# Performance work log

Measured on AMD Instinct MI355X. Metric: run time of the kernel, lower is better.

Reference implementation:

```python
import jax, jax.numpy as jnp
import numpy as np
from jax import lax

VOCAB = 2048
HID = 1024
BATCH = 64
SEQ = 256

def setup_inputs() -> dict:
    key = jax.random.key(0)
    ks = jax.random.split(key, 6)
    s = 0.02
    return {
        "X": jax.random.randint(ks[0], (BATCH, SEQ), 0, VOCAB),
        # gate weights stacked as [f, i, o, c_tilde] along output dim (same math as 4 separate Linears)
        "W1": jax.random.normal(ks[1], (VOCAB + HID, 4 * HID), jnp.float32) * s,
        "b1": jnp.zeros((4 * HID,), jnp.float32),
        "W2": jax.random.normal(ks[2], (HID + HID, 4 * HID), jnp.float32) * s,
        "b2": jnp.zeros((4 * HID,), jnp.float32),
        "W3": jax.random.normal(ks[3], (HID + HID, 4 * HID), jnp.float32) * s,
        "b3": jnp.zeros((4 * HID,), jnp.float32),
        "Wout": jax.random.normal(ks[4], (HID, VOCAB), jnp.float32) * s,
        "bout": jnp.zeros((VOCAB,), jnp.float32),
    }

def _cell(x, h, c, W, b):
    # concat(x, h) @ [Wf|Wi|Wo|Wc] + b -> split into 4 gates
    g = jnp.concatenate([x, h], axis=1) @ W + b
    f, i, o, ct = jnp.split(g, 4, axis=1)
    c = jax.nn.sigmoid(f) * c + jax.nn.sigmoid(i) * jnp.tanh(ct)
    h = jax.nn.sigmoid(o) * jnp.tanh(c)
    return h, c

def reference(X, W1, b1, W2, b2, W3, b3, Wout, bout):
    Xoh = jax.nn.one_hot(X.T, VOCAB, dtype=jnp.float32)  # [T, B, V]
    z = jnp.zeros((BATCH, HID), jnp.float32)
    init = (z, z, z, z, z, z)

    def step(carry, x):
        h1, c1, h2, c2, h3, c3 = carry
        h1, c1 = _cell(x, h1, c1, W1, b1)
        h2, c2 = _cell(h1, h2, c2, W2, b2)
        h3, c3 = _cell(h2, h3, c3, W3, b3)
        y = h3 @ Wout + bout  # [B, V]
        return (h1, c1, h2, c2, h3, c3), y

    carry, ys = lax.scan(step, init, Xoh)
    out = ys.reshape(SEQ * BATCH, VOCAB)  # == torch.cat(outputs, dim=0)
    h1, c1, h2, c2, h3, c3 = carry
    return (out, h1, c1, h2, c2, h3, c3)
```

## Files before the change

kernel.cpp:

```cpp
#include <hip/hip_runtime.h>
#include <hip/hip_cooperative_groups.h>
#include <math.h>

namespace cg = cooperative_groups;

#define NBLK 256
#define NTHR 512
#define HID  1024
#define NB   64
#define SEQL 256
#define VOC  2048
#define G4   4096

typedef __attribute__((ext_vector_type(8))) short bf16x8;
typedef __attribute__((ext_vector_type(4))) float f32x4;

__device__ __forceinline__ float sigm(float x) { return 1.0f / (1.0f + expf(-x)); }

#define OFF_P1 0u
#define OFF_P2 16777216u
#define OFF_P3 50331648u
#define OFF_PY 83886080u
#define OFF_H  92274688u
#define OFF_C  93847552u
#define WS_NEED 94633984ull

struct SmemF {
    short bbuf[2][32768];
    float tile[64 * 33];
    f32x4 red[8][64];
    int   tok[64];
};

__device__ void prepack_gate(uint32_t* __restrict__ img, const float* __restrict__ W,
                             int row0, int ta)
{
    for (int s = threadIdx.x; s < 16384; s += NTHR) {
        const int b4 = s * 4;
        const int plane = b4 >> 15;
        const int bb = b4 & 32767;
        const int L = bb >> 10;
        const int r = (bb & 1023) ^ ((L & 7) << 4);
        const int k = r >> 1;
        const int col = (L >> 3) * 1024 + ta * 8 + (L & 7);
        const float v0 = W[(size_t)(row0 + k) * G4 + col];
        const float v1 = W[(size_t)(row0 + k + 1) * G4 + col];
        uint32_t u;
        if (plane == 0) {
            u = (__float_as_uint(v0) >> 16) | (__float_as_uint(v1) & 0xFFFF0000u);
        } else {
            const float l0 = v0 - __uint_as_float(__float_as_uint(v0) & 0xFFFF0000u);
            const float l1 = v1 - __uint_as_float(__float_as_uint(v1) & 0xFFFF0000u);
            u = (__float_as_uint(l0) >> 16) | (__float_as_uint(l1) & 0xFFFF0000u);
        }
        img[s] = u;
    }
}

__device__ void prepack_y(uint32_t* __restrict__ img, const float* __restrict__ Wo,
                          int row0, int ty)
{
    for (int s = threadIdx.x; s < 8192; s += NTHR) {
        const int b4 = s * 4;
        const int plane = b4 >> 14;
        const int bb = b4 & 16383;
        const int L = bb >> 10;
        const int r = (bb & 1023) ^ ((L & 7) << 4);
        const int k = r >> 1;
        const int col = ty * 16 + L;
        const float v0 = Wo[(size_t)(row0 + k) * VOC + col];
        const float v1 = Wo[(size_t)(row0 + k + 1) * VOC + col];
        uint32_t u;
        if (plane == 0) {
            u = (__float_as_uint(v0) >> 16) | (__float_as_uint(v1) & 0xFFFF0000u);
        } else {
            const float l0 = v0 - __uint_as_float(__float_as_uint(v0) & 0xFFFF0000u);
            const float l1 = v1 - __uint_as_float(__float_as_uint(v1) & 0xFFFF0000u);
            u = (__float_as_uint(l0) >> 16) | (__float_as_uint(l1) & 0xFFFF0000u);
        }
        img[s] = u;
    }
}

template<int NCH, bool TWOSEG>
__device__ __forceinline__ void gemm_gate(SmemF* sm, const char* __restrict__ pack,
    const short* __restrict__ A0, const short* __restrict__ A1)
{
    const int tid = threadIdx.x;
    const int w = tid >> 6, lane = tid & 63;
    const int mt = w >> 1, nt = w & 1;
    const int c16 = lane & 15, g = lane >> 4;
    const int Lcol = nt * 16 + c16;
    const int swz = (Lcol & 7) << 4;

    f32x4 acc = {0.f, 0.f, 0.f, 0.f};
    uint4 st[8];

    #pragma unroll
    for (int i = 0; i < 8; ++i)
        st[i] = *(const uint4*)(pack + (i * NTHR + tid) * 16);
    #pragma unroll
    for (int i = 0; i < 8; ++i)
        *(uint4*)((char*)sm->bbuf[0] + (i * NTHR + tid) * 16) = st[i];
    __syncthreads();

    #pragma unroll
    for (int ch = 0; ch < NCH; ++ch) {
        if (ch + 1 < NCH) {
            const char* src = pack + (size_t)(ch + 1) * 65536;
            #pragma unroll
            for (int i = 0; i < 8; ++i)
                st[i] = *(const uint4*)(src + (i * NTHR + tid) * 16);
        }
        const short* Aseg = (TWOSEG && ch >= 2) ? A1 : A0;
        const int kk0 = (TWOSEG ? (ch & 1) : ch) * 512;
        const short* ah = Aseg + (size_t)(mt * 16 + c16) * 1024 + kk0 + g * 8;
        const short* al = ah + 65536;
        const char* bb = (const char*)sm->bbuf[ch & 1];
        #pragma unroll
        for (int ks = 0; ks < 16; ++ks) {
            const int bofs = (Lcol * 1024 + ks * 64 + g * 16) ^ swz;
            const bf16x8 b_h = *(const bf16x8*)(bb + bofs);
            const bf16x8 b_l = *(const bf16x8*)(bb + 32768 + bofs);
            const bf16x8 a_h = *(const bf16x8*)(ah + ks * 32);
            const bf16x8 a_l = *(const bf16x8*)(al + ks * 32);
            acc = __builtin_amdgcn_mfma_f32_16x16x32_bf16(a_h, b_h, acc, 0, 0, 0);
            acc = __builtin_amdgcn_mfma_f32_16x16x32_bf16(a_l, b_h, acc, 0, 0, 0);
            acc = __builtin_amdgcn_mfma_f32_16x16x32_bf16(a_h, b_l, acc, 0, 0, 0);
        }
        if (ch + 1 < NCH) {
            #pragma unroll
            for (int i = 0; i < 8; ++i)
                *(uint4*)((char*)sm->bbuf[(ch + 1) & 1] + (i * NTHR + tid) * 16) = st[i];
        }
        __syncthreads();
    }
    const int r0 = mt * 16 + g * 4;
    sm->tile[(r0 + 0) * 33 + Lcol] = acc[0];
    sm->tile[(r0 + 1) * 33 + Lcol] = acc[1];
    sm->tile[(r0 + 2) * 33 + Lcol] = acc[2];
    sm->tile[(r0 + 3) * 33 + Lcol] = acc[3];
    __syncthreads();
}

__device__ __forceinline__ void gemm_y(SmemF* sm, const char* __restrict__ pack,
                                       const short* __restrict__ A0)
{
    const int tid = threadIdx.x;
    const int w = tid >> 6, lane = tid & 63;
    const int mt = w >> 1, kh = w & 1;
    const int c16 = lane & 15, g = lane >> 4;
    const int swz = (c16 & 7) << 4;

    f32x4 acc = {0.f, 0.f, 0.f, 0.f};
    uint4 st[4];
    #pragma unroll
    for (int i = 0; i < 4; ++i)
        st[i] = *(const uint4*)(pack + (i * NTHR + tid) * 16);
    #pragma unroll
    for (int i = 0; i < 4; ++i)
        *(uint4*)((char*)sm->bbuf[0] + (i * NTHR + tid) * 16) = st[i];
    __syncthreads();

    #pragma unroll
    for (int ch = 0; ch < 2; ++ch) {
        if (ch == 0) {
            const char* src = pack + 32768;
            #pragma unroll
            for (int i = 0; i < 4; ++i)
                st[i] = *(const uint4*)(src + (i * NTHR + tid) * 16);
        }
        const int kk0 = ch * 512 + kh * 256;
        const short* ah = A0 + (size_t)(mt * 16 + c16) * 1024 + kk0 + g * 8;
        const short* al = ah + 65536;
        const char* bb = (const char*)sm->bbuf[ch & 1];
        #pragma unroll
        for (int ks = 0; ks < 8; ++ks) {
            const int koff = kh * 256 + ks * 32 + g * 8;
            const int bofs = (c16 * 1024 + koff * 2) ^ swz;
            const bf16x8 b_h = *(const bf16x8*)(bb + bofs);
            const bf16x8 b_l = *(const bf16x8*)(bb + 16384 + bofs);
            const bf16x8 a_h = *(const bf16x8*)(ah + ks * 32);
            const bf16x8 a_l = *(const bf16x8*)(al + ks * 32);
            acc = __builtin_amdgcn_mfma_f32_16x16x32_bf16(a_h, b_h, acc, 0, 0, 0);
            acc = __builtin_amdgcn_mfma_f32_16x16x32_bf16(a_l, b_h, acc, 0, 0, 0);
            acc = __builtin_amdgcn_mfma_f32_16x16x32_bf16(a_h, b_l, acc, 0, 0, 0);
        }
        if (ch == 0) {
            #pragma unroll
            for (int i = 0; i < 4; ++i)
                *(uint4*)((char*)sm->bbuf[1] + (i * NTHR + tid) * 16) = st[i];
        }
        __syncthreads();
    }
    sm->red[w][lane] = acc;
    __syncthreads();
}

__device__ __forceinline__ void gate_epi(SmemF* sm, const float* __restrict__ bias,
    const float* __restrict__ Wgather, float* __restrict__ cst,
    short* __restrict__ Hout, int ta)
{
    const int tid = threadIdx.x;
    const int m = tid & 63, u = tid >> 6;
    const int hb = ta * 8 + u;
    const float* tl = sm->tile + m * 33;
    float f  = tl[u]      + bias[hb];
    float i  = tl[8 + u]  + bias[1024 + hb];
    float o  = tl[16 + u] + bias[2048 + hb];
    float ct = tl[24 + u] + bias[3072 + hb];
    if (Wgather) {
        const float* wr = Wgather + (size_t)sm->tok[m] * G4 + hb;
        f += wr[0]; i += wr[1024]; o += wr[2048]; ct += wr[3072];
    }
    float* cp = cst + hb * 64 + m;
    const float cn = sigm(f) * (*cp) + sigm(i) * tanhf(ct);
    *cp = cn;
    const float h = sigm(o) * tanhf(cn);
    const uint32_t uh = __float_as_uint(h);
    const float lof = h - __uint_as_float(uh & 0xFFFF0000u);
    Hout[m * 1024 + hb] = (short)(uh >> 16);
    Hout[65536 + m * 1024 + hb] = (short)(__float_as_uint(lof) >> 16);
}

__device__ __forceinline__ void y_epi(SmemF* sm, int t, const float* __restrict__ bo,
                                      int vc0, float* __restrict__ out)
{
    const int tid = threadIdx.x;
    const int c = tid & 15, m0 = tid >> 4;
    #pragma unroll
    for (int hh = 0; hh < 2; ++hh) {
        const int m = m0 + hh * 32;
        const int mt = m >> 4, mr = m & 15;
        const int l = ((mr >> 2) << 4) | c;
        const int i = mr & 3;
        const float v = sm->red[mt * 2][l][i] + sm->red[mt * 2 + 1][l][i] + bo[vc0 + c];
        __builtin_nontemporal_store(v, out + ((size_t)t * NB + m) * VOC + vc0 + c);
    }
    __syncthreads();
}

__device__ __forceinline__ float recon(const short* __restrict__ Hp, size_t idx)
{
    return __uint_as_float(((uint32_t)(uint16_t)Hp[idx]) << 16)
         + __uint_as_float(((uint32_t)(uint16_t)Hp[65536 + idx]) << 16);
}

__global__ __launch_bounds__(NTHR, 2) void lstm3_v3(
    const int*   __restrict__ X,
    const float* __restrict__ W1, const float* __restrict__ b1,
    const float* __restrict__ W2, const float* __restrict__ b2,
    const float* __restrict__ W3, const float* __restrict__ b3,
    const float* __restrict__ Wo, const float* __restrict__ bo,
    float* __restrict__ out, char* __restrict__ wsb)
{
    cg::grid_group grid = cg::this_grid();
    __shared__ SmemF sm;

    const int tid = threadIdx.x, blk = blockIdx.x;
    const bool grpA = blk < 128;
    const int bb_ = grpA ? blk : blk - 128;
    const int ta = (bb_ & 7) * 16 + (bb_ >> 3);

    uint32_t* zr = (uint32_t*)(wsb + OFF_H);
    for (int i = blk * NTHR + tid; i < 589824; i += NBLK * NTHR) zr[i] = 0u;

    if (grpA) {
        for (int ch = 0; ch < 2; ++ch)
            prepack_gate((uint32_t*)(wsb + OFF_P1 + (size_t)ta * 131072 + ch * 65536),
                         W1, VOC + ch * 512, ta);
        for (int ch = 0; ch < 4; ++ch)
            prepack_gate((uint32_t*)(wsb + OFF_P3 + (size_t)ta * 262144 + ch * 65536),
                         W3, ch * 512, ta);
    } else {
        for (int ch = 0; ch < 4; ++ch)
            prepack_gate((uint32_t*)(wsb + OFF_P2 + (size_t)ta * 262144 + ch * 65536),
                         W2, ch * 512, ta);
        for (int ch = 0; ch < 2; ++ch)
            prepack_y((uint32_t*)(wsb + OFF_PY + (size_t)ta * 65536 + ch * 32768),
                      Wo, ch * 512, ta);
    }
    grid.sync();

    short* H = (short*)(wsb + OFF_H);
    float* C = (float*)(wsb + OFF_C);
    #define HP(l_, s_) (H + ((l_) * 2 + (s_)) * 131072)

    for (int s = 0; s <= SEQL + 2; ++s) {
        if (tid < 64 && s < SEQL) sm.tok[tid] = X[tid * SEQL + s];

        if (grpA) {
            if (s < SEQL) {
                const int sl = s & 1;
                gemm_gate<2, false>(&sm, wsb + OFF_P1 + (size_t)ta * 131072,
                                    HP(0, sl ^ 1), nullptr);
                gate_epi(&sm, b1, W1, C + 0 * 65536, HP(0, sl), ta);
            }
            if (s >= 2 && s <= SEQL + 1) {
                const int t = s - 2, sl = t & 1;
                gemm_gate<4, true>(&sm, wsb + OFF_P3 + (size_t)ta * 262144,
                                   HP(1, sl), HP(2, sl ^ 1));
                gate_epi(&sm, b3, nullptr, C + 2 * 65536, HP(2, sl), ta);
            }
        } else {
            if (s >= 1 && s <= SEQL) {
                const int t = s - 1, sl = t & 1;
                gemm_gate<4, true>(&sm, wsb + OFF_P2 + (size_t)ta * 262144,
                                   HP(0, sl), HP(1, sl ^ 1));
                gate_epi(&sm, b2, nullptr, C + 1 * 65536, HP(1, sl), ta);
            }
            if (s >= 3) {
                const int t = s - 3, sl = t & 1;
                gemm_y(&sm, wsb + OFF_PY + (size_t)ta * 65536, HP(2, sl));
                y_epi(&sm, t, bo, ta * 16, out);
            }
        }
        grid.sync();
    }

    {
        const int m = tid & 63, u = tid >> 6;
        const size_t base = (size_t)SEQL * NB * VOC;
        const size_t idx = (size_t)m * 1024 + ta * 8 + u;
        const int cu = (ta * 8 + u) * 64 + m;
        if (grpA) {
            out[base + idx]               = recon(HP(0, 1), idx);
            out[base + 65536 + idx]       = C[0 * 65536 + cu];
            out[base + 4 * 65536 + idx]   = recon(HP(2, 1), idx);
            out[base + 5 * 65536 + idx]   = C[2 * 65536 + cu];
        } else {
            out[base + 2 * 65536 + idx]   = recon(HP(1, 1), idx);
            out[base + 3 * 65536 + idx]   = C[1 * 65536 + cu];
        }
    }
    #undef HP
}

#define STG_STRIDE 520

struct SmemFB {
    short stg_hi[16 * STG_STRIDE];
    short stg_lo[16 * STG_STRIDE];
    f32x4 red[8][64];
    float tile[64 * 17];
    float cst[3 * 4 * 64];
    int   tok[64];
};

template<int KTOT, int MTILES>
__device__ void fb_gemm(SmemFB* sm, const float* __restrict__ W, int ldw, int wrow0,
                        const short* __restrict__ Ahi0, const short* __restrict__ Alo0,
                        const short* __restrict__ Ahi1, const short* __restrict__ Alo1,
                        bool gatecols, int cb, int mbase)
{
    constexpr int WPM = 8 / MTILES;
    constexpr int RPW = 512 / WPM;
    constexpr int KS  = RPW / 32;
    constexpr int NCH = KTOT / 512;

    const int tid = threadIdx.x;
    const int l   = tid & 63, w = tid >> 6;
    const int c16 = l & 15,  g = l >> 4;
    const int mt  = w / WPM, sub = w % WPM;
    const int sg  = tid & 3, kp  = tid >> 2;
    const int gc  = gatecols ? (sg * HID + cb) : (cb + sg * 4);

    f32x4 acc = {0.f, 0.f, 0.f, 0.f};

    for (int ch = 0; ch < NCH; ++ch) {
        #pragma unroll
        for (int rep = 0; rep < 2; ++rep) {
            const int kpair = kp + rep * 128;
            const int row   = wrow0 + ch * 512 + kpair * 2;
            const float4 w0 = *(const float4*)(W + (size_t)row * ldw + gc);
            const float4 w1 = *(const float4*)(W + (size_t)(row + 1) * ldw + gc);
            const float* a = (const float*)&w0;
            const float* b = (const float*)&w1;
            #pragma unroll
            for (int c = 0; c < 4; ++c) {
                const uint32_t ua = __float_as_uint(a[c]);
                const uint32_t ub = __float_as_uint(b[c]);
                const uint32_t hi = (ub & 0xFFFF0000u) | (ua >> 16);
                const float la = a[c] - __uint_as_float(ua & 0xFFFF0000u);
                const float lb = b[c] - __uint_as_float(ub & 0xFFFF0000u);
                const uint32_t lo = (__float_as_uint(lb) & 0xFFFF0000u)
                                  | (__float_as_uint(la) >> 16);
                const int off = (sg * 4 + c) * STG_STRIDE + kpair * 2;
                *(uint32_t*)&sm->stg_hi[off] = hi;
                *(uint32_t*)&sm->stg_lo[off] = lo;
            }
        }
        __syncthreads();

        const int kglob0 = ch * 512;
        const short* ahi = (KTOT == 2048 && kglob0 >= 1024) ? Ahi1 : Ahi0;
        const short* alo = (KTOT == 2048 && kglob0 >= 1024) ? Alo1 : Alo0;
        const int kk0 = kglob0 & 1023;
        const size_t arow = (size_t)(mbase + mt * 16 + c16) * HID;
        const short* ah = ahi + arow + kk0 + sub * RPW + g * 8;
        const short* al = alo + arow + kk0 + sub * RPW + g * 8;
        const short* bh = sm->stg_hi + c16 * STG_STRIDE + sub * RPW + g * 8;
        const short* bl = sm->stg_lo + c16 * STG_STRIDE + sub * RPW + g * 8;
        #pragma unroll
        for (int ks = 0; ks < KS; ++ks) {
            const bf16x8 a_hi = *(const bf16x8*)(ah + ks * 32);
            const bf16x8 a_lo = *(const bf16x8*)(al + ks * 32);
            const bf16x8 b_hi = *(const bf16x8*)(bh + ks * 32);
            const bf16x8 b_lo = *(const bf16x8*)(bl + ks * 32);
            acc = __builtin_amdgcn_mfma_f32_16x16x32_bf16(a_hi, b_hi, acc, 0, 0, 0);
            acc = __builtin_amdgcn_mfma_f32_16x16x32_bf16(a_lo, b_hi, acc, 0, 0, 0);
            acc = __builtin_amdgcn_mfma_f32_16x16x32_bf16(a_hi, b_lo, acc, 0, 0, 0);
        }
        __syncthreads();
    }

    sm->red[w][l] = acc;
    __syncthreads();
    if (sub == 0) {
        #pragma unroll
        for (int j = 1; j < WPM; ++j) {
            const f32x4 o = sm->red[w + j][l];
            acc[0] += o[0]; acc[1] += o[1]; acc[2] += o[2]; acc[3] += o[3];
        }
        const int r0 = mt * 16 + (l >> 4) * 4;
        sm->tile[(r0 + 0) * 17 + c16] = acc[0];
        sm->tile[(r0 + 1) * 17 + c16] = acc[1];
        sm->tile[(r0 + 2) * 17 + c16] = acc[2];
        sm->tile[(r0 + 3) * 17 + c16] = acc[3];
    }
    __syncthreads();
}

__device__ void fb_gate_epi(SmemFB* sm, int layer, const float* __restrict__ bias,
                            const float* __restrict__ W1gather, int hjb,
                            short* __restrict__ Hhi, short* __restrict__ Hlo)
{
    const int tid = threadIdx.x;
    if (tid < 256) {
        const int m = tid & 63, dh = tid >> 6;
        float f  = sm->tile[m * 17 + dh]       + bias[hjb + dh];
        float i  = sm->tile[m * 17 + 4 + dh]   + bias[HID + hjb + dh];
        float o  = sm->tile[m * 17 + 8 + dh]   + bias[2 * HID + hjb + dh];
        float ct = sm->tile[m * 17 + 12 + dh]  + bias[3 * HID + hjb + dh];
        if (W1gather) {
            const float* wr = W1gather + (size_t)sm->tok[m] * G4 + hjb + dh;
            f += wr[0]; i += wr[HID]; o += wr[2 * HID]; ct += wr[3 * HID];
        }
        const int ci = (layer * 4 + dh) * 64 + m;
        const float cn = sigm(f) * sm->cst[ci] + sigm(i) * tanhf(ct);
        sm->cst[ci] = cn;
        const float h = sigm(o) * tanhf(cn);
        const uint32_t uh = __float_as_uint(h);
        const float hiF = __uint_as_float(uh & 0xFFFF0000u);
        const float loV = h - hiF;
        const size_t idx = (size_t)m * HID + hjb + dh;
        Hhi[idx] = (short)(uh >> 16);
        Hlo[idx] = (short)(__float_as_uint(loV) >> 16);
    }
}

__device__ void fb_y_epi(SmemFB* sm, int t, const float* __restrict__ bo,
                         int vc0, int mh, float* __restrict__ out)
{
    const int tid = threadIdx.x;
    const int mloc = tid >> 4, c = tid & 15;
    const float v = sm->tile[mloc * 17 + c] + bo[vc0 + c];
    const int m = mh * 32 + mloc;
    __builtin_nontemporal_store(v, out + ((size_t)t * NB + m) * VOC + vc0 + c);
}

__global__ __launch_bounds__(NTHR, 1) void lstm3_fb(
    const int*   __restrict__ X,
    const float* __restrict__ W1, const float* __restrict__ b1,
    const float* __restrict__ W2, const float* __restrict__ b2,
    const float* __restrict__ W3, const float* __restrict__ b3,
    const float* __restrict__ Wo, const float* __restrict__ bo,
    float* __restrict__ out, short* __restrict__ hws)
{
    cg::grid_group grid = cg::this_grid();
    __shared__ SmemFB sm;

    const int tid = threadIdx.x;
    const int blk = blockIdx.x;
    const int tile = (blk & 7) * 32 + (blk >> 3);
    const int hjb  = tile * 4;
    const int q    = blk >> 3;
    const int ytile = (blk & 7) * 16 + (q & 15);
    const int mh    = q >> 4;
    const int vc0   = ytile * 16;

    uint32_t* wz = (uint32_t*)hws;
    for (int i = blk * NTHR + tid; i < 6 * 65536; i += NBLK * NTHR) wz[i] = 0u;
    for (int i = tid; i < 768; i += NTHR) sm.cst[i] = 0.f;
    grid.sync();

    #define HHI(l_, s_) (hws + ((l_) * 2 + (s_)) * 131072)
    #define HLO(l_, s_) (hws + ((l_) * 2 + (s_)) * 131072 + 65536)

    for (int s = 0; s <= SEQL + 2; ++s) {
        if (s < SEQL && tid < 64) sm.tok[tid] = X[tid * SEQL + s];

        if (s < SEQL) {
            const int t = s, sl = t & 1, sp = sl ^ 1;
            fb_gemm<1024, 4>(&sm, W1, G4, VOC, HHI(0, sp), HLO(0, sp),
                             nullptr, nullptr, true, hjb, 0);
            fb_gate_epi(&sm, 0, b1, W1, hjb, HHI(0, sl), HLO(0, sl));
        }
        if (s >= 1 && s <= SEQL) {
            const int t = s - 1, sl = t & 1, sp = sl ^ 1;
            fb_gemm<2048, 4>(&sm, W2, G4, 0, HHI(0, sl), HLO(0, sl),
                             HHI(1, sp), HLO(1, sp), true, hjb, 0);
            fb_gate_epi(&sm, 1, b2, nullptr, hjb, HHI(1, sl), HLO(1, sl));
        }
        if (s >= 2 && s <= SEQL + 1) {
            const int t = s - 2, sl = t & 1, sp = sl ^ 1;
            fb_gemm<2048, 4>(&sm, W3, G4, 0, HHI(1, sl), HLO(1, sl),
                             HHI(2, sp), HLO(2, sp), true, hjb, 0);
            fb_gate_epi(&sm, 2, b3, nullptr, hjb, HHI(2, sl), HLO(2, sl));
        }
        if (s >= 3) {
            const int t = s - 3, sl = t & 1;
            fb_gemm<1024, 2>(&sm, Wo, VOC, 0, HHI(2, sl), HLO(2, sl),
                             nullptr, nullptr, false, vc0, mh * 32);
            fb_y_epi(&sm, t, bo, vc0, mh, out);
        }
        grid.sync();
    }

    if (tid < 256) {
        const int m = tid & 63, dh = tid >> 6;
        const size_t base = (size_t)SEQL * NB * VOC;
        #pragma unroll
        for (int lyr = 0; lyr < 3; ++lyr) {
            const short* hh = HHI(lyr, 1);
            const short* hl = HLO(lyr, 1);
            const size_t idx = (size_t)m * HID + hjb + dh;
            const float h = __uint_as_float(((uint32_t)(uint16_t)hh[idx]) << 16)
                          + __uint_as_float(((uint32_t)(uint16_t)hl[idx]) << 16);
            out[base + (size_t)(2 * lyr) * 65536 + idx] = h;
            out[base + (size_t)(2 * lyr + 1) * 65536 + idx] =
                sm.cst[(lyr * 4 + dh) * 64 + m];
        }
    }
    #undef HHI
    #undef HLO
}

extern "C" void kernel_launch(void* const* d_in, const int* in_sizes, int n_in,
                              void* d_out, int out_size, void* d_ws, size_t ws_size,
                              hipStream_t stream)
{
    const int*   X  = (const int*)  d_in[0];
    const float* W1 = (const float*)d_in[1];
    const float* b1 = (const float*)d_in[2];
    const float* W2 = (const float*)d_in[3];
    const float* b2 = (const float*)d_in[4];
    const float* W3 = (const float*)d_in[5];
    const float* b3 = (const float*)d_in[6];
    const float* Wo = (const float*)d_in[7];
    const float* bo = (const float*)d_in[8];
    float* out = (float*)d_out;

    if (ws_size >= WS_NEED) {
        char* wsb = (char*)d_ws;
        void* args[] = { &X, &W1, &b1, &W2, &b2, &W3, &b3, &Wo, &bo, &out, &wsb };
        hipLaunchCooperativeKernel((const void*)lstm3_v3,
                                   dim3(NBLK), dim3(NTHR), args, 0, stream);
    } else {
        short* hws = (short*)d_ws;
        void* args[] = { &X, &W1, &b1, &W2, &b2, &W3, &b3, &Wo, &bo, &out, &hws };
        hipLaunchCooperativeKernel((const void*)lstm3_fb,
                                   dim3(NBLK), dim3(NTHR), args, 0, stream);
    }
}
```

Measured before the change: 24.07 ms.

## Replace grid.sync with flag-based barrier and split-K gate GEMM with relaxed atomics

Replaces the cooperative-groups grid.sync per timestep with a custom centralized flag barrier, where block 0 gathers per-block flags and releases the others. Hidden-state reads and writes become relaxed agent-scope atomics so cross-block data stays coherent without heavier fences. The gate GEMM is restructured so each wave computes two N-tiles over half the K range, then reduces through shared memory, with A operands loaded up front. The gate epilogue packs two outputs per thread. The intent is to cut per-step barrier latency. The risks are memory-ordering bugs, since relaxed ordering is used, and extra shared-memory reduction cost.

```diff
diff --git a/kernel.cpp b/kernel.cpp
--- a/kernel.cpp
+++ b/kernel.cpp
@@ -14,6 +14,7 @@
 
 typedef __attribute__((ext_vector_type(8))) short bf16x8;
 typedef __attribute__((ext_vector_type(4))) float f32x4;
+typedef unsigned long long ULL;
 
 __device__ __forceinline__ float sigm(float x) { return 1.0f / (1.0f + expf(-x)); }
 
@@ -23,14 +24,43 @@
 #define OFF_PY 83886080u
 #define OFF_H  92274688u
 #define OFF_C  93847552u
-#define WS_NEED 94633984ull
+#define OFF_FLG 94633984u
+#define WS_NEED 94638080ull
 
 struct SmemF {
     short bbuf[2][32768];
     float tile[64 * 33];
-    f32x4 red[8][64];
+    f32x4 redA[8][64];
+    f32x4 redB[8][64];
     int   tok[64];
 };
+
+union UB { ULL u[2]; bf16x8 v; };
+
+__device__ __forceinline__ void gbar(int* flags, int e) {
+    asm volatile("s_waitcnt vmcnt(0) lgkmcnt(0)" ::: "memory");
+    __syncthreads();
+    if (blockIdx.x == 0) {
+        const int t = threadIdx.x;
+        if (t >= 1 && t < NBLK) {
+            while ((int)((unsigned)__hip_atomic_load(&flags[t * 4], __ATOMIC_RELAXED,
+                          __HIP_MEMORY_SCOPE_AGENT) - (unsigned)e) < 0)
+                __builtin_amdgcn_s_sleep(8);
+        }
+        __syncthreads();
+        if (t == 0)
+            __hip_atomic_store(&flags[0], e, __ATOMIC_RELAXED, __HIP_MEMORY_SCOPE_AGENT);
+    } else {
+        if (threadIdx.x == 0) {
+            __hip_atomic_store(&flags[blockIdx.x * 4], e, __ATOMIC_RELAXED,
+                               __HIP_MEMORY_SCOPE_AGENT);
+            while ((int)((unsigned)__hip_atomic_load(&flags[0], __ATOMIC_RELAXED,
+                          __HIP_MEMORY_SCOPE_AGENT) - (unsigned)e) < 0)
+                __builtin_amdgcn_s_sleep(8);
+        }
+        __syncthreads();
+    }
+}
 
 __device__ void prepack_gate(uint32_t* __restrict__ img, const float* __restrict__ W,
                              int row0, int ta)
@@ -88,12 +118,11 @@
 {
     const int tid = threadIdx.x;
     const int w = tid >> 6, lane = tid & 63;
-    const int mt = w >> 1, nt = w & 1;
+    const int mt = w >> 1, kh = w & 1;
     const int c16 = lane & 15, g = lane >> 4;
-    const int Lcol = nt * 16 + c16;
-    const int swz = (Lcol & 7) << 4;
-
-    f32x4 acc = {0.f, 0.f, 0.f, 0.f};
+    const int swz = (c16 & 7) << 4;
+
+    f32x4 acc0 = {0.f, 0.f, 0.f, 0.f}, acc1 = {0.f, 0.f, 0.f, 0.f};
     uint4 st[8];
 
     #pragma unroll
@@ -113,20 +142,37 @@
                 st[i] = *(const uint4*)(src + (i * NTHR + tid) * 16);
         }
         const short* Aseg = (TWOSEG && ch >= 2) ? A1 : A0;
-        const int kk0 = (TWOSEG ? (ch & 1) : ch) * 512;
-        const short* ah = Aseg + (size_t)(mt * 16 + c16) * 1024 + kk0 + g * 8;
-        const short* al = ah + 65536;
+        const int kk0 = (TWOSEG ? (ch & 1) : ch) * 512 + kh * 256;
+        const short* ap = Aseg + (size_t)(mt * 16 + c16) * 1024 + kk0 + g * 8;
+        ULL ahx[8][2], alx[8][2];
+        #pragma unroll
+        for (int ks = 0; ks < 8; ++ks) {
+            const ULL* ph = (const ULL*)(ap + ks * 32);
+            const ULL* pl = (const ULL*)(ap + 65536 + ks * 32);
+            ahx[ks][0] = __hip_atomic_load(ph,     __ATOMIC_RELAXED, __HIP_MEMORY_SCOPE_AGENT);
+            ahx[ks][1] = __hip_atomic_load(ph + 1, __ATOMIC_RELAXED, __HIP_MEMORY_SCOPE_AGENT);
+            alx[ks][0] = __hip_atomic_load(pl,     __ATOMIC_RELAXED, __HIP_MEMORY_SCOPE_AGENT);
+            alx[ks][1] = __hip_atomic_load(pl + 1, __ATOMIC_RELAXED, __HIP_MEMORY_SCOPE_AGENT);
+        }
         const char* bb = (const char*)sm->bbuf[ch & 1];
         #pragma unroll
-        for (int ks = 0; ks < 16; ++ks) {
-            const int bofs = (Lcol * 1024 + ks * 64 + g * 16) ^ swz;
-            const bf16x8 b_h = *(const bf16x8*)(bb + bofs);
-            const bf16x8 b_l = *(const bf16x8*)(bb + 32768 + bofs);
-            const bf16x8 a_h = *(const bf16x8*)(ah + ks * 32);
-            const bf16x8 a_l = *(const bf16x8*)(al + ks * 32);
-            acc = __builtin_amdgcn_mfma_f32_16x16x32_bf16(a_h, b_h, acc, 0, 0, 0);
-            acc = __builtin_amdgcn_mfma_f32_16x16x32_bf16(a_l, b_h, acc, 0, 0, 0);
-            acc = __builtin_amdgcn_mfma_f32_16x16x32_bf16(a_h, b_l, acc, 0, 0, 0);
+        for (int ks = 0; ks < 8; ++ks) {
+            UB a_h, a_l;
+            a_h.u[0] = ahx[ks][0]; a_h.u[1] = ahx[ks][1];
+            a_l.u[0] = alx[ks][0]; a_l.u[1] = alx[ks][1];
+            const int kb = kh * 512 + ks * 64 + g * 16;
+            const int b0 = (c16 * 1024 + kb) ^ swz;
+            const int b1 = ((16 + c16) * 1024 + kb) ^ swz;
+            const bf16x8 bh0 = *(const bf16x8*)(bb + b0);
+            const bf16x8 bl0 = *(const bf16x8*)(bb + 32768 + b0);
+            const bf16x8 bh1 = *(const bf16x8*)(bb + b1);
+            const bf16x8 bl1 = *(const bf16x8*)(bb + 32768 + b1);
+            acc0 = __builtin_amdgcn_mfma_f32_16x16x32_bf16(a_h.v, bh0, acc0, 0, 0, 0);
+            acc0 = __builtin_amdgcn_mfma_f32_16x16x32_bf16(a_l.v, bh0, acc0, 0, 0, 0);
+            acc0 = __builtin_amdgcn_mfma_f32_16x16x32_bf16(a_h.v, bl0, acc0, 0, 0, 0);
+            acc1 = __builtin_amdgcn_mfma_f32_16x16x32_bf16(a_h.v, bh1, acc1, 0, 0, 0);
+            acc1 = __builtin_amdgcn_mfma_f32_16x16x32_bf16(a_l.v, bh1, acc1, 0, 0, 0);
+            acc1 = __builtin_amdgcn_mfma_f32_16x16x32_bf16(a_h.v, bl1, acc1, 0, 0, 0);
         }
         if (ch + 1 < NCH) {
             #pragma unroll
@@ -135,11 +181,22 @@
         }
         __syncthreads();
     }
-    const int r0 = mt * 16 + g * 4;
-    sm->tile[(r0 + 0) * 33 + Lcol] = acc[0];
-    sm->tile[(r0 + 1) * 33 + Lcol] = acc[1];
-    sm->tile[(r0 + 2) * 33 + Lcol] = acc[2];
-    sm->tile[(r0 + 3) * 33 + Lcol] = acc[3];
+
+    sm->redA[w][lane] = acc0;
+    sm->redB[w][lane] = acc1;
+    __syncthreads();
+    if (kh == 0) {
+        const f32x4 o0 = sm->redA[w + 1][lane];
+        const f32x4 o1 = sm->redB[w + 1][lane];
+        #pragma unroll
+        for (int i2 = 0; i2 < 4; ++i2) { acc0[i2] += o0[i2]; acc1[i2] += o1[i2]; }
+        const int r0 = mt * 16 + g * 4;
+        #pragma unroll
+        for (int i2 = 0; i2 < 4; ++i2) {
+            sm->tile[(r0 + i2) * 33 + c16]      = acc0[i2];
+            sm->tile[(r0 + i2) * 33 + 16 + c16] = acc1[i2];
+        }
+    }
     __syncthreads();
 }
 
@@ -171,20 +228,30 @@
                 st[i] = *(const uint4*)(src + (i * NTHR + tid) * 16);
         }
         const int kk0 = ch * 512 + kh * 256;
-        const short* ah = A0 + (size_t)(mt * 16 + c16) * 1024 + kk0 + g * 8;
-        const short* al = ah + 65536;
+        const short* ap = A0 + (size_t)(mt * 16 + c16) * 1024 + kk0 + g * 8;
+        ULL ahx[8][2], alx[8][2];
+        #pragma unroll
+        for (int ks = 0; ks < 8; ++ks) {
+            const ULL* ph = (const ULL*)(ap + ks * 32);
+            const ULL* pl = (const ULL*)(ap + 65536 + ks * 32);
+            ahx[ks][0] = __hip_atomic_load(ph,     __ATOMIC_RELAXED, __HIP_MEMORY_SCOPE_AGENT);
+            ahx[ks][1] = __hip_atomic_load(ph + 1, __ATOMIC_RELAXED, __HIP_MEMORY_SCOPE_AGENT);
+            alx[ks][0] = __hip_atomic_load(pl,     __ATOMIC_RELAXED, __HIP_MEMORY_SCOPE_AGENT);
+            alx[ks][1] = __hip_atomic_load(pl + 1, __ATOMIC_RELAXED, __HIP_MEMORY_SCOPE_AGENT);
+        }
         const char* bb = (const char*)sm->bbuf[ch & 1];
         #pragma unroll
         for (int ks = 0; ks < 8; ++ks) {
-            const int koff = kh * 256 + ks * 32 + g * 8;
-            const int bofs = (c16 * 1024 + koff * 2) ^ swz;
-            const bf16x8 b_h = *(const bf16x8*)(bb + bofs);
-            const bf16x8 b_l = *(const bf16x8*)(bb + 16384 + bofs);
-            const bf16x8 a_h = *(const bf16x8*)(ah + ks * 32);
-            const bf16x8 a_l = *(const bf16x8*)(al + ks * 32);
-            acc = __builtin_amdgcn_mfma_f32_16x16x32_bf16(a_h, b_h, acc, 0, 0, 0);
-            acc = __builtin_amdgcn_mfma_f32_16x16x32_bf16(a_l, b_h, acc, 0, 0, 0);
-            acc = __builtin_amdgcn_mfma_f32_16x16x32_bf16(a_h, b_l, acc, 0, 0, 0);
+            UB a_h, a_l;
+            a_h.u[0] = ahx[ks][0]; a_h.u[1] = ahx[ks][1];
+            a_l.u[0] = alx[ks][0]; a_l.u[1] = alx[ks][1];
+            const int kb = kh * 512 + ks * 64 + g * 16;
+            const int b0 = (c16 * 1024 + kb) ^ swz;
+            const bf16x8 bh0 = *(const bf16x8*)(bb + b0);
+            const bf16x8 bl0 = *(const bf16x8*)(bb + 16384 + b0);
+            acc = __builtin_amdgcn_mfma_f32_16x16x32_bf16(a_h.v, bh0, acc, 0, 0, 0);
+            acc = __builtin_amdgcn_mfma_f32_16x16x32_bf16(a_l.v, bh0, acc, 0, 0, 0);
+            acc = __builtin_amdgcn_mfma_f32_16x16x32_bf16(a_h.v, bl0, acc, 0, 0, 0);
         }
         if (ch == 0) {
             #pragma unroll
@@ -193,7 +260,7 @@
         }
         __syncthreads();
     }
-    sm->red[w][lane] = acc;
+    sm->redA[w][lane] = acc;
     __syncthreads();
 }
 
@@ -202,25 +269,37 @@
     short* __restrict__ Hout, int ta)
 {
     const int tid = threadIdx.x;
-    const int m = tid & 63, u = tid >> 6;
-    const int hb = ta * 8 + u;
-    const float* tl = sm->tile + m * 33;
-    float f  = tl[u]      + bias[hb];
-    float i  = tl[8 + u]  + bias[1024 + hb];
-    float o  = tl[16 + u] + bias[2048 + hb];
-    float ct = tl[24 + u] + bias[3072 + hb];
-    if (Wgather) {
-        const float* wr = Wgather + (size_t)sm->tok[m] * G4 + hb;
-        f += wr[0]; i += wr[1024]; o += wr[2048]; ct += wr[3072];
-    }
-    float* cp = cst + hb * 64 + m;
-    const float cn = sigm(f) * (*cp) + sigm(i) * tanhf(ct);
-    *cp = cn;
-    const float h = sigm(o) * tanhf(cn);
-    const uint32_t uh = __float_as_uint(h);
-    const float lof = h - __uint_as_float(uh & 0xFFFF0000u);
-    Hout[m * 1024 + hb] = (short)(uh >> 16);
-    Hout[65536 + m * 1024 + hb] = (short)(__float_as_uint(lof) >> 16);
+    if (tid < 256) {
+        const int m = tid & 63, up = tid >> 6;
+        const float* tl = sm->tile + m * 33;
+        uint32_t hiw = 0, low = 0;
+        #pragma unroll
+        for (int q = 0; q < 2; ++q) {
+            const int u = up * 2 + q;
+            const int hb = ta * 8 + u;
+            float f  = tl[u]      + bias[hb];
+            float i  = tl[8 + u]  + bias[1024 + hb];
+            float o  = tl[16 + u] + bias[2048 + hb];
+            float ct = tl[24 + u] + bias[3072 + hb];
+            if (Wgather) {
+                const float* wr = Wgather + (size_t)sm->tok[m] * G4 + hb;
+                f += wr[0]; i += wr[1024]; o += wr[2048]; ct += wr[3072];
+            }
+            float* cp = cst + hb * 64 + m;
+            const float cn = sigm(f) * (*cp) + sigm(i) * tanhf(ct);
+            *cp = cn;
+            const float h = sigm(o) * tanhf(cn);
+            const uint32_t uh = __float_as_uint(h);
+            const float lof = h - __uint_as_float(uh & 0xFFFF0000u);
+            hiw |= (uh >> 16) << (16 * q);
+            low |= (__float_as_uint(lof) >> 16) << (16 * q);
+        }
+        const int si = m * 1024 + ta * 8 + up * 2;
+        __hip_atomic_store((uint32_t*)(Hout + si), hiw,
+                           __ATOMIC_RELAXED, __HIP_MEMORY_SCOPE_AGENT);
+        __hip_atomic_store((uint32_t*)(Hout + 65536 + si), low,
+                           __ATOMIC_RELAXED, __HIP_MEMORY_SCOPE_AGENT);
+    }
 }
 
 __device__ __forceinline__ void y_epi(SmemF* sm, int t, const float* __restrict__ bo,
@@ -234,19 +313,13 @@
         const int mt = m >> 4, mr = m & 15;
         const int l = ((mr >> 2) << 4) | c;
         const int i = mr & 3;
-        const float v = sm->red[mt * 2][l][i] + sm->red[mt * 2 + 1][l][i] + bo[vc0 + c];
+        const float v = sm->redA[mt * 2][l][i] + sm->redA[mt * 2 + 1][l][i] + bo[vc0 + c];
         __builtin_nontemporal_store(v, out + ((size_t)t * NB + m) * VOC + vc0 + c);
     }
     __syncthreads();
 }
 
-__device__ __forceinline__ float recon(const short* __restrict__ Hp, size_t idx)
-{
-    return __uint_as_float(((uint32_t)(uint16_t)Hp[idx]) << 16)
-         + __uint_as_float(((uint32_t)(uint16_t)Hp[65536 + idx]) << 16);
-}
-
-__global__ __launch_bounds__(NTHR, 2) void lstm3_v3(
+__global__ __launch_bounds__(NTHR, 2) void lstm3_v5(
     const int*   __restrict__ X,
     const float* __restrict__ W1, const float* __restrict__ b1,
     const float* __restrict__ W2, const float* __restrict__ b2,
@@ -259,11 +332,25 @@
 
     const int tid = threadIdx.x, blk = blockIdx.x;
     const bool grpA = blk < 128;
-    const int bb_ = grpA ? blk : blk - 128;
-    const int ta = (bb_ & 7) * 16 + (bb_ >> 3);
-
-    uint32_t* zr = (uint32_t*)(wsb + OFF_H);
-    for (int i = blk * NTHR + tid; i < 589824; i += NBLK * NTHR) zr[i] = 0u;
+    const int bidx = grpA ? blk : blk - 128;
+    const int ta = (bidx & 7) * 16 + (bidx >> 3);
+    int* flags = (int*)(wsb + OFF_FLG);
+
+    if (tid == 0)
+        __hip_atomic_store(&flags[blk * 4], 0, __ATOMIC_RELAXED, __HIP_MEMORY_SCOPE_AGENT);
+
+    uint32_t* hz = (uint32_t*)(wsb + OFF_H);
+    for (int i = blk * NTHR + tid; i < 393216; i += NBLK * NTHR) hz[i] = 0u;
+    float* C = (float*)(wsb + OFF_C);
+    if (grpA) {
+        for (int i = tid; i < 512; i += NTHR) {
+            C[ta * 512 + i] = 0.f;
+            C[2 * 65536 + ta * 512 + i] = 0.f;
+        }
+    } else {
+        for (int i = tid; i < 512; i += NTHR)
+            C[65536 + ta * 512 + i] = 0.f;
+    }
 
     if (grpA) {
         for (int ch = 0; ch < 2; ++ch)
@@ -283,7 +370,6 @@
     grid.sync();
 
     short* H = (short*)(wsb + OFF_H);
-    float* C = (float*)(wsb + OFF_C);
     #define HP(l_, s_) (H + ((l_) * 2 + (s_)) * 131072)
 
     for (int s = 0; s <= SEQL + 2; ++s) {
@@ -294,7 +380,7 @@
                 const int sl = s & 1;
                 gemm_gate<2, false>(&sm, wsb + OFF_P1 + (size_t)ta * 131072,
                                     HP(0, sl ^ 1), nullptr);
-                gate_epi(&sm, b1, W1, C + 0 * 65536, HP(0, sl), ta);
+                gate_epi(&sm, b1, W1, C, HP(0, sl), ta);
             }
             if (s >= 2 && s <= SEQL + 1) {
                 const int t = s - 2, sl = t & 1;
@@ -307,7 +393,7 @@
                 const int t = s - 1, sl = t & 1;
                 gemm_gate<4, true>(&sm, wsb + OFF_P2 + (size_t)ta * 262144,
                                    HP(0, sl), HP(1, sl ^ 1));
-                gate_epi(&sm, b2, nullptr, C + 1 * 65536, HP(1, sl), ta);
+                gate_epi(&sm, b2, nullptr, C + 65536, HP(1, sl), ta);
             }
             if (s >= 3) {
                 const int t = s - 3, sl = t & 1;
@@ -315,22 +401,31 @@
                 y_epi(&sm, t, bo, ta * 16, out);
             }
         }
-        grid.sync();
-    }
-
-    {
-        const int m = tid & 63, u = tid >> 6;
+        gbar(flags, s + 1);
+    }
+
+    if (tid < 256) {
+        const int m = tid & 63, up = tid >> 6;
         const size_t base = (size_t)SEQL * NB * VOC;
-        const size_t idx = (size_t)m * 1024 + ta * 8 + u;
-        const int cu = (ta * 8 + u) * 64 + m;
-        if (grpA) {
-            out[base + idx]               = recon(HP(0, 1), idx);
-            out[base + 65536 + idx]       = C[0 * 65536 + cu];
-            out[base + 4 * 65536 + idx]   = recon(HP(2, 1), idx);
-            out[base + 5 * 65536 + idx]   = C[2 * 65536 + cu];
-        } else {
-            out[base + 2 * 65536 + idx]   = recon(HP(1, 1), idx);
-            out[base + 3 * 65536 + idx]   = C[1 * 65536 + cu];
+        const size_t si = (size_t)m * 1024 + ta * 8 + up * 2;
+        const int cu = (ta * 8 + up * 2) * 64 + m;
+        #pragma unroll
+        for (int pick = 0; pick < 2; ++pick) {
+            const int lyr = grpA ? (pick ? 2 : 0) : 1;
+            if (!grpA && pick) break;
+            const short* hp = HP(lyr, 1);
+            const uint32_t hw = __hip_atomic_load((const uint32_t*)(hp + si),
+                                  __ATOMIC_RELAXED, __HIP_MEMORY_SCOPE_AGENT);
+            const uint32_t lw = __hip_atomic_load((const uint32_t*)(hp + 65536 + si),
+                                  __ATOMIC_RELAXED, __HIP_MEMORY_SCOPE_AGENT);
+            const size_t ob = base + (size_t)(2 * lyr) * 65536 + si;
+            out[ob]     = __uint_as_float((hw & 0xFFFFu) << 16)
+                        + __uint_as_float((lw & 0xFFFFu) << 16);
+            out[ob + 1] = __uint_as_float(hw & 0xFFFF0000u)
+                        + __uint_as_float(lw & 0xFFFF0000u);
+            const float* Cl = C + lyr * 65536;
+            out[base + (size_t)(2 * lyr + 1) * 65536 + si]     = Cl[cu];
+            out[base + (size_t)(2 * lyr + 1) * 65536 + si + 1] = Cl[cu + 64];
         }
     }
     #undef HP
@@ -564,7 +659,7 @@
     if (ws_size >= WS_NEED) {
         char* wsb = (char*)d_ws;
         void* args[] = { &X, &W1, &b1, &W2, &b2, &W3, &b3, &Wo, &bo, &out, &wsb };
-        hipLaunchCooperativeKernel((const void*)lstm3_v3,
+        hipLaunchCooperativeKernel((const void*)lstm3_v5,
                                    dim3(NBLK), dim3(NTHR), args, 0, stream);
     } else {
         short* hws = (short*)d_ws;
```

Measured after the change: 24.13 ms. Within noise of the previous version (+0.3%).
